# Optimization experiments

Hardware: AMD Instinct MI355X
Metric: run time of the kernel (lower is better)

Reference implementation:

```python
import jax, jax.numpy as jnp
import numpy as np

NEG_SLOPE = 0.2

def gat_conv(x, edge, W, att_src, att_dst, bias, heads, out_ch, concat):
    # x: [N, F_in], edge: [2, E] (self-loops already included)
    N = x.shape[0]
    src, dst = edge[0], edge[1]
    h = (x @ W).reshape(N, heads, out_ch)                     # [N, H, C]
    a_src = jnp.sum(h * att_src, axis=-1)                     # [N, H]
    a_dst = jnp.sum(h * att_dst, axis=-1)                     # [N, H]
    e = jax.nn.leaky_relu(a_src[src] + a_dst[dst], NEG_SLOPE)  # [E, H]
    # segment softmax over incoming edges of each dst node
    e_max = jax.ops.segment_max(e, dst, num_segments=N)       # [N, H]
    e_exp = jnp.exp(e - e_max[dst])                           # [E, H]
    denom = jax.ops.segment_sum(e_exp, dst, num_segments=N)   # [N, H]
    alpha = e_exp / denom[dst]                                # [E, H]
    msg = h[src] * alpha[:, :, None]                          # [E, H, C]
    out = jax.ops.segment_sum(msg, dst, num_segments=N)       # [N, H, C]
    if concat:
        out = out.reshape(N, heads * out_ch)
    else:
        out = out.mean(axis=1)
    return out + bias


def setup_inputs() -> dict:
    key = jax.random.key(0)
    ks = jax.random.split(key, 10)
    N, E = 50000, 1600000
    F_in, H, C1, n_cls = 256, 4, 64, 40
    x = jax.random.normal(ks[0], (N, F_in), dtype=jnp.float32)
    edge_index = jax.random.randint(ks[1], (2, E), 0, N, dtype=jnp.int64)
    s1 = 1.0 / np.sqrt(F_in)
    s2 = 1.0 / np.sqrt(H * C1)
    return {
        "x": x,
        "edge_index": edge_index,
        "W1": jax.random.normal(ks[2], (F_in, H * C1), dtype=jnp.float32) * s1,
        "att_src1": jax.random.normal(ks[3], (H, C1), dtype=jnp.float32) * s2,
        "att_dst1": jax.random.normal(ks[4], (H, C1), dtype=jnp.float32) * s2,
        "b1": jnp.zeros((H * C1,), dtype=jnp.float32),
        "W2": jax.random.normal(ks[5], (H * C1, n_cls), dtype=jnp.float32) * s2,
        "att_src2": jax.random.normal(ks[6], (1, n_cls), dtype=jnp.float32) * 0.1,
        "att_dst2": jax.random.normal(ks[7], (1, n_cls), dtype=jnp.float32) * 0.1,
        "b2": jnp.zeros((n_cls,), dtype=jnp.float32),
    }


def reference(x, edge_index, W1, att_src1, att_dst1, b1, W2, att_src2, att_dst2, b2):
    N = x.shape[0]
    # PyG GATConv adds self-loops by default
    loops = jnp.arange(N, dtype=edge_index.dtype)
    edge = jnp.concatenate([edge_index, jnp.stack([loops, loops])], axis=1)
    # dropout is identity in eval mode
    h = gat_conv(x, edge, W1, att_src1, att_dst1, b1, heads=4, out_ch=64, concat=True)
    h = jax.nn.elu(h)
    out = gat_conv(h, edge, W2, att_src2, att_dst2, b2, heads=1, out_ch=40, concat=False)
    return out
```

## Files before the change

### kernel.cpp

```cpp
#include <hip/hip_runtime.h>
#include <hip/hip_bf16.h>

typedef short bf16x8 __attribute__((ext_vector_type(8)));
typedef float f32x4 __attribute__((ext_vector_type(4)));
typedef float f32x2 __attribute__((ext_vector_type(2)));
typedef unsigned short u16x8 __attribute__((ext_vector_type(8)));

#define CHUNK 4096
#define BCAP 16384

__device__ __forceinline__ float wred_sum(float v) {
  #pragma unroll
  for (int off = 32; off > 0; off >>= 1)
    v += __shfl_xor(v, off, 64);
  return v;
}
__device__ __forceinline__ float b2f(unsigned short u) {
  union { unsigned int i; float f; } x;
  x.i = ((unsigned int)u) << 16;
  return x.f;
}
__device__ __forceinline__ unsigned short f2bu(float f) {
  __hip_bfloat16 b = __float2bfloat16(f);
  return *(unsigned short*)&b;
}
__device__ __forceinline__ void pkfma(f32x2& acc, f32x2 v, f32x2 w) {
  asm("v_pk_fma_f32 %0, %1, %2, %0" : "+v"(acc) : "v"(v), "v"(w));
}
__device__ __forceinline__ void qfma(f32x2* acc2, unsigned int u, f32x2 wp) {
  f32x2 a, b;
  a[0] = (float)(u & 0xFFu);         a[1] = (float)((u >> 8) & 0xFFu);
  b[0] = (float)((u >> 16) & 0xFFu); b[1] = (float)(u >> 24);
  pkfma(acc2[0], a, wp);
  pkfma(acc2[1], b, wp);
}
__device__ __forceinline__ void bffma(f32x2& acc, unsigned int up, f32x2 wp) {
  union { unsigned int i; float f; } lo, hi;
  lo.i = up << 16; hi.i = up & 0xFFFF0000u;
  f32x2 v; v[0] = lo.f; v[1] = hi.f;
  pkfma(acc, v, wp);
}
__device__ __forceinline__ float ldf(const void* p, long long i, int is16) {
  return is16 ? __bfloat162float(((const __hip_bfloat16*)p)[i])
              : ((const float*)p)[i];
}
__device__ __forceinline__ int edge_at(const int* e, long long idx, int is64) {
  return is64 ? (int)((const long long*)e)[idx] : e[idx];
}

__global__ void detect_kernel(const int* __restrict__ edge, int n_edge_check,
                              const unsigned int* __restrict__ xw, int n_x_check,
                              int* __restrict__ flag,
                              int* __restrict__ bcursor, int NB) {
  __shared__ int s_nz, s_cnt, s_tot;
  int tid = threadIdx.x;
  for (int b = tid; b < NB; b += 256) bcursor[b] = b * BCAP;
  if (tid == 0) { s_nz = 0; s_cnt = 0; s_tot = 0; }
  __syncthreads();
  int nz = 0;
  for (int k = tid; k < n_edge_check; k += 256)
    if (edge[2 * k + 1] != 0) nz = 1;
  if (nz) atomicOr(&s_nz, 1);
  int c = 0, t = 0;
  for (int k = tid; k < n_x_check; k += 256) {
    unsigned int w = xw[k];
    if (w == 0u) continue;
    t++;
    unsigned int e = (w >> 7) & 0xFFu;
    if (e >= 100u && e <= 150u) c++;
  }
  atomicAdd(&s_cnt, c);
  atomicAdd(&s_tot, t);
  __syncthreads();
  if (tid == 0) {
    flag[0] = (s_nz == 0) ? 1 : 0;
    flag[1] = (s_cnt * 10 > s_tot * 6) ? 1 : 0;
  }
}

__global__ __launch_bounds__(256) void partition_kernel(
    const int* __restrict__ edge, int E, int N, const int* __restrict__ flag,
    int* __restrict__ bcursor, unsigned int* __restrict__ part, int NB) {
  __shared__ int cnt[1024];
  __shared__ int loff[1025];
  __shared__ int gpos[1024];
  __shared__ int lcur[1024];
  __shared__ unsigned int staged[CHUNK];
  __shared__ int staged_addr[CHUNK];
  __shared__ int s[256];
  __shared__ int rbase;
  int tid = threadIdx.x;
  long long base = (long long)blockIdx.x * CHUNK;
  long long total = (long long)E + N;
  int maxa = NB * BCAP - 1;
  int here = (int)min((long long)CHUNK, total - base);
  for (int b = tid; b < NB; b += 256) cnt[b] = 0;
  if (tid == 0) rbase = 0;
  __syncthreads();
  int is64 = flag[0];
  int myb[16];
  unsigned int myp[16];
  #pragma unroll
  for (int j = 0; j < 16; j++) {
    long long i = base + j * 256 + tid;
    myb[j] = -1;
    if (i < total) {
      int d, sv;
      if (i < E) {
        sv = edge_at(edge, i, is64);
        d = edge_at(edge, (long long)E + i, is64);
      } else {
        sv = d = (int)(i - E);
      }
      d = min(max(d, 0), N - 1);
      sv = min(max(sv, 0), N - 1);
      myb[j] = d >> 8;
      myp[j] = ((unsigned int)(d & 255) << 24) | (unsigned int)sv;
      atomicAdd(&cnt[myb[j]], 1);
    }
  }
  __syncthreads();
  for (int c0 = 0; c0 < NB; c0 += 256) {
    int idx = c0 + tid;
    int v = (idx < NB) ? cnt[idx] : 0;
    s[tid] = v;
    __syncthreads();
    for (int off = 1; off < 256; off <<= 1) {
      int t = (tid >= off) ? s[tid - off] : 0;
      __syncthreads();
      s[tid] += t;
      __syncthreads();
    }
    int mb = rbase;
    if (idx < NB) loff[idx] = mb + s[tid] - v;
    __syncthreads();
    if (tid == 0) rbase = mb + s[255];
    __syncthreads();
  }
  __syncthreads();
  for (int b = tid; b < NB; b += 256) {
    int c = cnt[b];
    gpos[b] = c ? atomicAdd(&bcursor[b], c) : 0;
    lcur[b] = loff[b];
  }
  __syncthreads();
  #pragma unroll
  for (int j = 0; j < 16; j++) {
    if (myb[j] >= 0) {
      int b = myb[j];
      int slot = atomicAdd(&lcur[b], 1);
      staged[slot] = myp[j];
      staged_addr[slot] = min(gpos[b] + (slot - loff[b]), maxa);
    }
  }
  __syncthreads();
  for (int i = tid; i < here; i += 256)
    part[staged_addr[i]] = staged[i];
}

__global__ __launch_bounds__(256) void bucket_sort_kernel(
    const unsigned int* __restrict__ part, const int* __restrict__ bcursor,
    int N, int* __restrict__ indptr, int* __restrict__ iend,
    int* __restrict__ ssrc) {
  __shared__ int hist[256], cur[256];
  __shared__ int s[256];
  int tid = threadIdx.x;
  int b = blockIdx.x;
  int begin = b * BCAP, end = bcursor[b];
  hist[tid] = 0;
  __syncthreads();
  for (int i = begin + tid; i < end; i += 256)
    atomicAdd(&hist[part[i] >> 24], 1);
  __syncthreads();
  int v = hist[tid];
  s[tid] = v;
  __syncthreads();
  for (int off = 1; off < 256; off <<= 1) {
    int t = (tid >= off) ? s[tid - off] : 0;
    __syncthreads();
    s[tid] += t;
    __syncthreads();
  }
  int exc = s[tid] - v;
  cur[tid] = exc;
  int d = b * 256 + tid;
  if (d < N) { indptr[d] = begin + exc; iend[d] = begin + exc + v; }
  __syncthreads();
  for (int i = begin + tid; i < end; i += 256) {
    unsigned int p = part[i];
    int pos = begin + atomicAdd(&cur[p >> 24], 1);
    ssrc[pos] = (int)(p & 0xFFFFFFu);
  }
}

__global__ void prep_kernel(const void* __restrict__ x, __hip_bfloat16* __restrict__ xb,
                            long long n_valid4, long long nconv4,
                            const void* __restrict__ W1v, const void* __restrict__ W2v,
                            __hip_bfloat16* __restrict__ Wt1, __hip_bfloat16* __restrict__ Wt2,
                            int F, int HC, int C2, int C2p,
                            const int* __restrict__ dflag) {
  int f16 = dflag[1];
  long long i = blockIdx.x * 256LL + threadIdx.x;
  if (i < nconv4) {
    ushort4 o;
    if (i < n_valid4) {
      if (f16) {
        o = ((const ushort4*)x)[i];
      } else {
        float4 v = ((const float4*)x)[i];
        o.x = f2bu(v.x); o.y = f2bu(v.y); o.z = f2bu(v.z); o.w = f2bu(v.w);
      }
    } else {
      o.x = o.y = o.z = o.w = 0;
    }
    ((ushort4*)xb)[i] = o;
    return;
  }
  long long j = i - nconv4;
  int n1 = HC * F;
  if (j < n1) {
    int idx = (int)j;
    int n = idx / F, k = idx - n * F;
    Wt1[idx] = __float2bfloat16(ldf(W1v, (long long)k * HC + n, f16));
  } else {
    int jj = (int)(j - n1);
    if (jj >= C2p * HC) return;
    int n = jj / HC, k = jj - n * HC;
    float v = (n < C2) ? ldf(W2v, (long long)k * C2 + n, f16) : 0.f;
    Wt2[jj] = __float2bfloat16(v);
  }
}

__global__ __launch_bounds__(256) void mfma_gemm_kernel(
    const __hip_bfloat16* __restrict__ A, const __hip_bfloat16* __restrict__ BtT,
    __hip_bfloat16* __restrict__ Cb,
    const void* __restrict__ attS, const void* __restrict__ attD,
    float* __restrict__ aS, float* __restrict__ aD,
    float2* __restrict__ aSq, int att_stride,
    int M, int Nout, int K, int quant,
    unsigned char* __restrict__ h1q,
    const int* __restrict__ dflag) {
  int f16 = dflag[1];
  int tid = threadIdx.x;
  int w = tid >> 6, l = tid & 63;
  int m_lane = l & 15, q = l >> 4;
  int row0 = blockIdx.y * 64, col0 = blockIdx.x * 64;
  const __hip_bfloat16* Arow = A + (long long)(row0 + w * 16 + m_lane) * K + q * 8;
  const __hip_bfloat16* Brow = BtT + (long long)(col0 + m_lane) * K + q * 8;
  f32x4 acc[4] = {};
  #pragma unroll 4
  for (int k0 = 0; k0 < K; k0 += 32) {
    bf16x8 af = *(const bf16x8*)(Arow + k0);
    #pragma unroll
    for (int t = 0; t < 4; t++) {
      bf16x8 bf = *(const bf16x8*)(Brow + (long long)t * 16 * K + k0);
      acc[t] = __builtin_amdgcn_mfma_f32_16x16x32_bf16(af, bf, acc[t], 0, 0, 0);
    }
  }
  #pragma unroll
  for (int r = 0; r < 4; r++) {
    int gr = row0 + w * 16 + q * 4 + r;
    float ps = 0.f, pd = 0.f, vmax = 0.f;
    #pragma unroll
    for (int t = 0; t < 4; t++) {
      int gc = col0 + t * 16 + m_lane;
      float v = acc[t][r];
      if (gc < Nout) {
        ps += v * ldf(attS, gc, f16);
        pd += v * ldf(attD, gc, f16);
        vmax = fmaxf(vmax, fabsf(v));
        if (!quant && gr < M) Cb[(long long)gr * Nout + gc] = __float2bfloat16(v);
      }
    }
    #pragma unroll
    for (int off = 1; off < 16; off <<= 1) {
      ps += __shfl_xor(ps, off, 64);
      pd += __shfl_xor(pd, off, 64);
      vmax = fmaxf(vmax, __shfl_xor(vmax, off, 64));
    }
    if (quant && gr < M) {
      float qinv = (vmax > 0.f) ? 127.f / vmax : 0.f;
      #pragma unroll
      for (int t = 0; t < 4; t++) {
        int gc = col0 + t * 16 + m_lane;
        h1q[(long long)gr * 256 + gc] =
            (unsigned char)(__float2int_rn(acc[t][r] * qinv) + 128);
      }
      if (m_lane == 0) {
        float2 sq; sq.x = ps; sq.y = vmax * (1.f / 127.f);
        aSq[(long long)gr * att_stride + blockIdx.x] = sq;
      }
    }
    if (m_lane == 0 && gr < M) {
      if (!quant) aS[(long long)gr * att_stride + blockIdx.x] = ps;
      aD[(long long)gr * att_stride + blockIdx.x] = pd;
    }
  }
}

__global__ __launch_bounds__(256) void aggregate1_kernel(
    const int* __restrict__ indptr, const int* __restrict__ iend,
    const int* __restrict__ ssrc,
    const unsigned char* __restrict__ h1q, const float2* __restrict__ a_sq,
    const float* __restrict__ a_dst, const void* __restrict__ b1,
    __hip_bfloat16* __restrict__ h2b, int N, const int* __restrict__ dflag) {
  int f16 = dflag[1];
  int w = threadIdx.x >> 6, l = threadIdx.x & 63;
  int d = blockIdx.x * 4 + w;
  if (d >= N) return;
  int q = l >> 4;
  int e16 = l & 15;
  int hb = (l & 12) << 2;
  int chb = (l & 15) << 4;
  int begin = indptr[d], end = iend[d];
  float adst = a_dst[d * 4 + q];
  int s0 = ssrc[begin];
  float den = 0.f, accS = 0.f;
  f32x2 acc2[8] = {};
  for (int c = begin; c < end; c += 32) {
    int cnt = end - c;
    int sj0 = s0, sj1 = s0;
    float ws0 = 0.f, ws1 = 0.f;
    if (e16 < cnt) {
      sj0 = ssrc[c + e16];
      float2 t = a_sq[sj0 * 4 + q];
      float e = t.x + adst;
      e = (e > 0.f) ? e : 0.2f * e;
      float wj = __expf(e);
      den += wj; ws0 = wj * t.y;
    }
    if (e16 + 16 < cnt) {
      sj1 = ssrc[c + 16 + e16];
      float2 t = a_sq[sj1 * 4 + q];
      float e = t.x + adst;
      e = (e > 0.f) ? e : 0.2f * e;
      float wj = __expf(e);
      den += wj; ws1 = wj * t.y;
    }
    int m0 = cnt < 16 ? cnt : 16;
    int m1 = cnt - 16; m1 = m1 < 0 ? 0 : (m1 > 16 ? 16 : m1);
    int j0 = (m0 + 3) >> 2, j1 = (m1 + 3) >> 2;
    #pragma unroll 4
    for (int j = 0; j < j0; j++) {
      int idx = hb + 4 * j + q;
      int s = __shfl(sj0, idx, 64);
      float wt = __shfl(ws0, idx, 64);
      accS += wt;
      f32x2 wp; wp[0] = wt; wp[1] = wt;
      uint4 uv = *(const uint4*)(h1q + (long long)s * 256 + chb);
      qfma(&acc2[0], uv.x, wp);
      qfma(&acc2[2], uv.y, wp);
      qfma(&acc2[4], uv.z, wp);
      qfma(&acc2[6], uv.w, wp);
    }
    #pragma unroll 4
    for (int j = 0; j < j1; j++) {
      int idx = hb + 4 * j + q;
      int s = __shfl(sj1, idx, 64);
      float wt = __shfl(ws1, idx, 64);
      accS += wt;
      f32x2 wp; wp[0] = wt; wp[1] = wt;
      uint4 uv = *(const uint4*)(h1q + (long long)s * 256 + chb);
      qfma(&acc2[0], uv.x, wp);
      qfma(&acc2[2], uv.y, wp);
      qfma(&acc2[4], uv.z, wp);
      qfma(&acc2[6], uv.w, wp);
    }
  }
  float* af = (float*)acc2;
  #pragma unroll
  for (int i = 0; i < 16; i++) {
    af[i] += __shfl_xor(af[i], 16, 64);
    af[i] += __shfl_xor(af[i], 32, 64);
  }
  accS += __shfl_xor(accS, 16, 64);
  accS += __shfl_xor(accS, 32, 64);
  #pragma unroll
  for (int off = 1; off < 16; off <<= 1)
    den += __shfl_xor(den, off, 64);
  float deh = __shfl(den, hb, 64);
  float inv = 1.f / deh;
  if (l < 16) {
    u16x8 o0, o1;
    #pragma unroll
    for (int i = 0; i < 16; i++) {
      float v = (af[i] - 128.f * accS) * inv + ldf(b1, chb + i, f16);
      v = (v > 0.f) ? v : (__expf(v) - 1.f);
      if (i < 8) o0[i] = f2bu(v); else o1[i - 8] = f2bu(v);
    }
    u16x8* dst = (u16x8*)((unsigned short*)h2b + (long long)d * 256 + chb);
    dst[0] = o0;
    dst[1] = o1;
  }
}

__global__ __launch_bounds__(256) void aggregate2_kernel(
    const int* __restrict__ indptr, const int* __restrict__ iend,
    const int* __restrict__ ssrc,
    const __hip_bfloat16* __restrict__ gb, const float* __restrict__ a_src,
    const float* __restrict__ a_dst, const void* __restrict__ b2,
    void* __restrict__ out, int N, int C, const int* __restrict__ dflag) {
  int f16 = dflag[1];
  int w = threadIdx.x >> 6, l = threadIdx.x & 63;
  int d = blockIdx.x * 4 + w;
  if (d >= N) return;
  int begin = indptr[d], end = iend[d];
  float adst = a_dst[d];
  int eg = l / 10;
  int cq = l - eg * 10;
  bool act = (eg < 6);
  int s0 = ssrc[begin];
  float den = 0.f;
  f32x2 acc01 = {0.f, 0.f}, acc23 = {0.f, 0.f};
  for (int c = begin; c < end; c += 64) {
    int cnt = min(64, end - c);
    int sj = s0;
    float wj = 0.f;
    if (l < cnt) {
      sj = ssrc[c + l];
      float e = a_src[sj] + adst;
      e = (e > 0.f) ? e : 0.2f * e;
      wj = __expf(e);
    }
    den += wj;
    int jm = (cnt + 5) / 6;
    #pragma unroll 4
    for (int j = 0; j < jm; j++) {
      int idx = 6 * j + eg;
      int s = __shfl(sj, idx & 63, 64);
      float wt = __shfl(wj, idx & 63, 64);
      if (!act || idx >= cnt) wt = 0.f;
      uint2 gv = *(const uint2*)((const unsigned short*)gb +
                                 (long long)s * C + 4 * cq);
      f32x2 wp; wp[0] = wt; wp[1] = wt;
      bffma(acc01, gv.x, wp);
      bffma(acc23, gv.y, wp);
    }
  }
  den = wred_sum(den);
  float inv = 1.f / den;
  float a0 = acc01[0], a1 = acc01[1], a2 = acc23[0], a3 = acc23[1];
  #pragma unroll
  for (int k = 1; k < 6; k++) {
    int srcl = cq + 10 * k;
    a0 += __shfl(acc01[0], srcl, 64);
    a1 += __shfl(acc01[1], srcl, 64);
    a2 += __shfl(acc23[0], srcl, 64);
    a3 += __shfl(acc23[1], srcl, 64);
  }
  if (l < 10) {
    float v0 = a0 * inv + ldf(b2, 4 * l + 0, f16);
    float v1 = a1 * inv + ldf(b2, 4 * l + 1, f16);
    float v2 = a2 * inv + ldf(b2, 4 * l + 2, f16);
    float v3 = a3 * inv + ldf(b2, 4 * l + 3, f16);
    long long o = (long long)d * C + 4 * l;
    if (f16) {
      ushort4 ov;
      ov.x = f2bu(v0); ov.y = f2bu(v1); ov.z = f2bu(v2); ov.w = f2bu(v3);
      *(ushort4*)((unsigned short*)out + o) = ov;
    } else {
      float4 ov;
      ov.x = v0; ov.y = v1; ov.z = v2; ov.w = v3;
      *(float4*)((float*)out + o) = ov;
    }
  }
}

extern "C" void kernel_launch(void* const* d_in, const int* in_sizes, int n_in,
                              void* d_out, int out_size, void* d_ws, size_t ws_size,
                              hipStream_t stream) {
  const void* x   = d_in[0];
  const int* edge = (const int*)d_in[1];
  const void* W1  = d_in[2];
  const void* as1 = d_in[3];
  const void* ad1 = d_in[4];
  const void* b1  = d_in[5];
  const void* W2  = d_in[6];
  const void* as2 = d_in[7];
  const void* ad2 = d_in[8];
  const void* b2  = d_in[9];

  const int F  = 256;
  const int HC = 256;
  const int N  = in_sizes[0] / F;
  const int E  = in_sizes[1] / 2;
  const int C2 = in_sizes[9];
  const int C2p = 64;
  const int total = E + N;
  const int NB = (N + 255) / 256;
  const int Mpad = ((N + 63) / 64) * 64;

  char* p = (char*)d_ws;
  auto alloc = [&](size_t bytes) -> void* {
    void* r = (void*)p;
    p += (bytes + 255) & ~(size_t)255;
    return r;
  };
  __hip_bfloat16* xb  = (__hip_bfloat16*)alloc((size_t)Mpad * F * 2);
  unsigned char*  h1q = (unsigned char*)alloc((size_t)Mpad * HC);
  __hip_bfloat16* h2b = (__hip_bfloat16*)alloc((size_t)Mpad * HC * 2);
  __hip_bfloat16* gb  = (__hip_bfloat16*)alloc((size_t)Mpad * C2 * 2);
  __hip_bfloat16* Wt1 = (__hip_bfloat16*)alloc((size_t)HC * F * 2);
  __hip_bfloat16* Wt2 = (__hip_bfloat16*)alloc((size_t)C2p * HC * 2);
  float2* a_sq1 = (float2*)alloc((size_t)N * 4 * 8);
  float* a_dst1 = (float*)alloc((size_t)N * 4 * 4);
  float* a_src2 = (float*)alloc((size_t)N * 4);
  float* a_dst2 = (float*)alloc((size_t)N * 4);
  unsigned int* part = (unsigned int*)alloc((size_t)NB * BCAP * 4);
  int* ssrc     = (int*)alloc((size_t)NB * BCAP * 4);
  int* bcursor  = (int*)alloc((size_t)NB * 4);
  int* indptr   = (int*)alloc((size_t)(N + 1) * 4);
  int* iend     = (int*)alloc((size_t)N * 4);
  int* flag     = (int*)alloc(256);

  detect_kernel<<<1, 256, 0, stream>>>(edge, E < 2048 ? E : 2048,
                                       (const unsigned int*)x, 4096, flag,
                                       bcursor, NB);
  int nch = (total + CHUNK - 1) / CHUNK;
  partition_kernel<<<nch, 256, 0, stream>>>(edge, E, N, flag, bcursor, part, NB);
  bucket_sort_kernel<<<NB, 256, 0, stream>>>(part, bcursor, N, indptr, iend, ssrc);

  long long nconv4 = (long long)Mpad * F / 4;
  long long nprep = nconv4 + (long long)HC * F + (long long)C2p * HC;
  prep_kernel<<<(int)((nprep + 255) / 256), 256, 0, stream>>>(
      x, xb, (long long)N * F / 4, nconv4, W1, W2, Wt1, Wt2, F, HC, C2, C2p, flag);

  dim3 g1(HC / 64, Mpad / 64);
  mfma_gemm_kernel<<<g1, 256, 0, stream>>>(xb, Wt1, nullptr,
                                           as1, ad1, nullptr, a_dst1, a_sq1, 4,
                                           N, HC, F, 1, h1q, flag);
  aggregate1_kernel<<<(N + 3) / 4, 256, 0, stream>>>(indptr, iend, ssrc, h1q, a_sq1,
                                                     a_dst1, b1, h2b, N, flag);

  dim3 g2(1, Mpad / 64);
  mfma_gemm_kernel<<<g2, 256, 0, stream>>>(h2b, Wt2, gb,
                                           as2, ad2, a_src2, a_dst2, nullptr, 1,
                                           N, C2, HC, 0, nullptr, flag);
  aggregate2_kernel<<<(N + 3) / 4, 256, 0, stream>>>(indptr, iend, ssrc, gb, a_src2, a_dst2,
                                                     b2, d_out, N, C2, flag);
}
```

Baseline: 373.3 us.

## Replace bucket partition sort with atomic CSR build and fuse x conversion into GEMM

The two-pass bucket partition and bucket sort are replaced by three kernels: a global atomic degree count, a per-block scan with an atomic block base, and an atomic-cursor scatter of source indices. The separate fp32-to-bf16 conversion pass over x is removed, and the first GEMM now loads fp32 rows and converts them to bf16 in registers. This cuts a full read and write of x plus the intermediate partition buffer. In exchange it adds global atomics on hot destinations and reads edges twice, and the CSR order becomes nondeterministic because blocks claim scan offsets through an atomic rather than in block order.

```diff
diff --git a/kernel.cpp b/kernel.cpp
--- a/kernel.cpp
+++ b/kernel.cpp
@@ -7,7 +7,6 @@
 typedef unsigned short u16x8 __attribute__((ext_vector_type(8)));
 
 #define CHUNK 4096
-#define BCAP 16384
 
 __device__ __forceinline__ float wred_sum(float v) {
   #pragma unroll
@@ -50,11 +49,9 @@
 
 __global__ void detect_kernel(const int* __restrict__ edge, int n_edge_check,
                               const unsigned int* __restrict__ xw, int n_x_check,
-                              int* __restrict__ flag,
-                              int* __restrict__ bcursor, int NB) {
+                              int* __restrict__ flag) {
   __shared__ int s_nz, s_cnt, s_tot;
   int tid = threadIdx.x;
-  for (int b = tid; b < NB; b += 256) bcursor[b] = b * BCAP;
   if (tid == 0) { s_nz = 0; s_cnt = 0; s_tot = 0; }
   __syncthreads();
   int nz = 0;
@@ -78,32 +75,56 @@
   }
 }
 
-__global__ __launch_bounds__(256) void partition_kernel(
+__global__ __launch_bounds__(256) void count_kernel(
     const int* __restrict__ edge, int E, int N, const int* __restrict__ flag,
-    int* __restrict__ bcursor, unsigned int* __restrict__ part, int NB) {
-  __shared__ int cnt[1024];
-  __shared__ int loff[1025];
-  __shared__ int gpos[1024];
-  __shared__ int lcur[1024];
-  __shared__ unsigned int staged[CHUNK];
-  __shared__ int staged_addr[CHUNK];
-  __shared__ int s[256];
-  __shared__ int rbase;
+    int* __restrict__ deg) {
   int tid = threadIdx.x;
   long long base = (long long)blockIdx.x * CHUNK;
   long long total = (long long)E + N;
-  int maxa = NB * BCAP - 1;
-  int here = (int)min((long long)CHUNK, total - base);
-  for (int b = tid; b < NB; b += 256) cnt[b] = 0;
-  if (tid == 0) rbase = 0;
-  __syncthreads();
   int is64 = flag[0];
-  int myb[16];
-  unsigned int myp[16];
   #pragma unroll
   for (int j = 0; j < 16; j++) {
     long long i = base + j * 256 + tid;
-    myb[j] = -1;
+    if (i < total) {
+      int d = (i < E) ? edge_at(edge, (long long)E + i, is64) : (int)(i - E);
+      d = min(max(d, 0), N - 1);
+      atomicAdd(&deg[d], 1);
+    }
+  }
+}
+
+__global__ __launch_bounds__(256) void scan_kernel(
+    const int* __restrict__ deg, int N, int* __restrict__ gcur,
+    int* __restrict__ indptr, int* __restrict__ iend, int* __restrict__ cursor) {
+  __shared__ int s[256];
+  __shared__ int base;
+  int tid = threadIdx.x;
+  int d = blockIdx.x * 256 + tid;
+  int v = (d < N) ? deg[d] : 0;
+  s[tid] = v;
+  __syncthreads();
+  for (int off = 1; off < 256; off <<= 1) {
+    int t = (tid >= off) ? s[tid - off] : 0;
+    __syncthreads();
+    s[tid] += t;
+    __syncthreads();
+  }
+  if (tid == 255) base = atomicAdd(gcur, s[255]);
+  __syncthreads();
+  int exc = base + s[tid] - v;
+  if (d < N) { indptr[d] = exc; iend[d] = exc + v; cursor[d] = exc; }
+}
+
+__global__ __launch_bounds__(256) void scatter_kernel(
+    const int* __restrict__ edge, int E, int N, const int* __restrict__ flag,
+    int* __restrict__ cursor, int* __restrict__ ssrc) {
+  int tid = threadIdx.x;
+  long long base = (long long)blockIdx.x * CHUNK;
+  long long total = (long long)E + N;
+  int is64 = flag[0];
+  #pragma unroll
+  for (int j = 0; j < 16; j++) {
+    long long i = base + j * 256 + tid;
     if (i < total) {
       int d, sv;
       if (i < E) {
@@ -114,116 +135,24 @@
       }
       d = min(max(d, 0), N - 1);
       sv = min(max(sv, 0), N - 1);
-      myb[j] = d >> 8;
-      myp[j] = ((unsigned int)(d & 255) << 24) | (unsigned int)sv;
-      atomicAdd(&cnt[myb[j]], 1);
-    }
-  }
-  __syncthreads();
-  for (int c0 = 0; c0 < NB; c0 += 256) {
-    int idx = c0 + tid;
-    int v = (idx < NB) ? cnt[idx] : 0;
-    s[tid] = v;
-    __syncthreads();
-    for (int off = 1; off < 256; off <<= 1) {
-      int t = (tid >= off) ? s[tid - off] : 0;
-      __syncthreads();
-      s[tid] += t;
-      __syncthreads();
-    }
-    int mb = rbase;
-    if (idx < NB) loff[idx] = mb + s[tid] - v;
-    __syncthreads();
-    if (tid == 0) rbase = mb + s[255];
-    __syncthreads();
-  }
-  __syncthreads();
-  for (int b = tid; b < NB; b += 256) {
-    int c = cnt[b];
-    gpos[b] = c ? atomicAdd(&bcursor[b], c) : 0;
-    lcur[b] = loff[b];
-  }
-  __syncthreads();
-  #pragma unroll
-  for (int j = 0; j < 16; j++) {
-    if (myb[j] >= 0) {
-      int b = myb[j];
-      int slot = atomicAdd(&lcur[b], 1);
-      staged[slot] = myp[j];
-      staged_addr[slot] = min(gpos[b] + (slot - loff[b]), maxa);
-    }
-  }
-  __syncthreads();
-  for (int i = tid; i < here; i += 256)
-    part[staged_addr[i]] = staged[i];
-}
-
-__global__ __launch_bounds__(256) void bucket_sort_kernel(
-    const unsigned int* __restrict__ part, const int* __restrict__ bcursor,
-    int N, int* __restrict__ indptr, int* __restrict__ iend,
-    int* __restrict__ ssrc) {
-  __shared__ int hist[256], cur[256];
-  __shared__ int s[256];
-  int tid = threadIdx.x;
-  int b = blockIdx.x;
-  int begin = b * BCAP, end = bcursor[b];
-  hist[tid] = 0;
-  __syncthreads();
-  for (int i = begin + tid; i < end; i += 256)
-    atomicAdd(&hist[part[i] >> 24], 1);
-  __syncthreads();
-  int v = hist[tid];
-  s[tid] = v;
-  __syncthreads();
-  for (int off = 1; off < 256; off <<= 1) {
-    int t = (tid >= off) ? s[tid - off] : 0;
-    __syncthreads();
-    s[tid] += t;
-    __syncthreads();
-  }
-  int exc = s[tid] - v;
-  cur[tid] = exc;
-  int d = b * 256 + tid;
-  if (d < N) { indptr[d] = begin + exc; iend[d] = begin + exc + v; }
-  __syncthreads();
-  for (int i = begin + tid; i < end; i += 256) {
-    unsigned int p = part[i];
-    int pos = begin + atomicAdd(&cur[p >> 24], 1);
-    ssrc[pos] = (int)(p & 0xFFFFFFu);
-  }
-}
-
-__global__ void prep_kernel(const void* __restrict__ x, __hip_bfloat16* __restrict__ xb,
-                            long long n_valid4, long long nconv4,
-                            const void* __restrict__ W1v, const void* __restrict__ W2v,
+      int pos = atomicAdd(&cursor[d], 1);
+      ssrc[pos] = sv;
+    }
+  }
+}
+
+__global__ void prep_kernel(const void* __restrict__ W1v, const void* __restrict__ W2v,
                             __hip_bfloat16* __restrict__ Wt1, __hip_bfloat16* __restrict__ Wt2,
                             int F, int HC, int C2, int C2p,
                             const int* __restrict__ dflag) {
   int f16 = dflag[1];
-  long long i = blockIdx.x * 256LL + threadIdx.x;
-  if (i < nconv4) {
-    ushort4 o;
-    if (i < n_valid4) {
-      if (f16) {
-        o = ((const ushort4*)x)[i];
-      } else {
-        float4 v = ((const float4*)x)[i];
-        o.x = f2bu(v.x); o.y = f2bu(v.y); o.z = f2bu(v.z); o.w = f2bu(v.w);
-      }
-    } else {
-      o.x = o.y = o.z = o.w = 0;
-    }
-    ((ushort4*)xb)[i] = o;
-    return;
-  }
-  long long j = i - nconv4;
+  int i = blockIdx.x * 256 + threadIdx.x;
   int n1 = HC * F;
-  if (j < n1) {
-    int idx = (int)j;
-    int n = idx / F, k = idx - n * F;
-    Wt1[idx] = __float2bfloat16(ldf(W1v, (long long)k * HC + n, f16));
+  if (i < n1) {
+    int n = i / F, k = i - n * F;
+    Wt1[i] = __float2bfloat16(ldf(W1v, (long long)k * HC + n, f16));
   } else {
-    int jj = (int)(j - n1);
+    int jj = i - n1;
     if (jj >= C2p * HC) return;
     int n = jj / HC, k = jj - n * HC;
     float v = (n < C2) ? ldf(W2v, (long long)k * C2 + n, f16) : 0.f;
@@ -232,25 +161,41 @@
 }
 
 __global__ __launch_bounds__(256) void mfma_gemm_kernel(
-    const __hip_bfloat16* __restrict__ A, const __hip_bfloat16* __restrict__ BtT,
+    const void* __restrict__ A, const __hip_bfloat16* __restrict__ BtT,
     __hip_bfloat16* __restrict__ Cb,
     const void* __restrict__ attS, const void* __restrict__ attD,
     float* __restrict__ aS, float* __restrict__ aD,
     float2* __restrict__ aSq, int att_stride,
-    int M, int Nout, int K, int quant,
+    int M, int Nout, int K, int quant, int amode,
     unsigned char* __restrict__ h1q,
     const int* __restrict__ dflag) {
   int f16 = dflag[1];
+  int af16 = amode | f16;
   int tid = threadIdx.x;
   int w = tid >> 6, l = tid & 63;
   int m_lane = l & 15, q = l >> 4;
   int row0 = blockIdx.y * 64, col0 = blockIdx.x * 64;
-  const __hip_bfloat16* Arow = A + (long long)(row0 + w * 16 + m_lane) * K + q * 8;
+  int arow = row0 + w * 16 + m_lane;
+  bool aok = (arow < M);
+  const __hip_bfloat16* Ab = (const __hip_bfloat16*)A + (long long)arow * K + q * 8;
+  const float* Af = (const float*)A + (long long)arow * K + q * 8;
   const __hip_bfloat16* Brow = BtT + (long long)(col0 + m_lane) * K + q * 8;
   f32x4 acc[4] = {};
   #pragma unroll 4
   for (int k0 = 0; k0 < K; k0 += 32) {
-    bf16x8 af = *(const bf16x8*)(Arow + k0);
+    bf16x8 af = {};
+    if (aok) {
+      if (af16) {
+        af = *(const bf16x8*)(Ab + k0);
+      } else {
+        float4 u0 = *(const float4*)(Af + k0);
+        float4 u1 = *(const float4*)(Af + k0 + 4);
+        af[0] = (short)f2bu(u0.x); af[1] = (short)f2bu(u0.y);
+        af[2] = (short)f2bu(u0.z); af[3] = (short)f2bu(u0.w);
+        af[4] = (short)f2bu(u1.x); af[5] = (short)f2bu(u1.y);
+        af[6] = (short)f2bu(u1.z); af[7] = (short)f2bu(u1.w);
+      }
+    }
     #pragma unroll
     for (int t = 0; t < 4; t++) {
       bf16x8 bf = *(const bf16x8*)(Brow + (long long)t * 16 * K + k0);
@@ -496,7 +441,6 @@
     p += (bytes + 255) & ~(size_t)255;
     return r;
   };
-  __hip_bfloat16* xb  = (__hip_bfloat16*)alloc((size_t)Mpad * F * 2);
   unsigned char*  h1q = (unsigned char*)alloc((size_t)Mpad * HC);
   __hip_bfloat16* h2b = (__hip_bfloat16*)alloc((size_t)Mpad * HC * 2);
   __hip_bfloat16* gb  = (__hip_bfloat16*)alloc((size_t)Mpad * C2 * 2);
@@ -506,36 +450,37 @@
   float* a_dst1 = (float*)alloc((size_t)N * 4 * 4);
   float* a_src2 = (float*)alloc((size_t)N * 4);
   float* a_dst2 = (float*)alloc((size_t)N * 4);
-  unsigned int* part = (unsigned int*)alloc((size_t)NB * BCAP * 4);
-  int* ssrc     = (int*)alloc((size_t)NB * BCAP * 4);
-  int* bcursor  = (int*)alloc((size_t)NB * 4);
-  int* indptr   = (int*)alloc((size_t)(N + 1) * 4);
+  int* deg      = (int*)alloc((size_t)(N + 64) * 4);
+  int* gcur     = deg + N;
+  int* cursor   = (int*)alloc((size_t)N * 4);
+  int* indptr   = (int*)alloc((size_t)N * 4);
   int* iend     = (int*)alloc((size_t)N * 4);
+  int* ssrc     = (int*)alloc((size_t)total * 4);
   int* flag     = (int*)alloc(256);
 
+  hipMemsetAsync(deg, 0, (size_t)(N + 64) * 4, stream);
   detect_kernel<<<1, 256, 0, stream>>>(edge, E < 2048 ? E : 2048,
-                                       (const unsigned int*)x, 4096, flag,
-                                       bcursor, NB);
+                                       (const unsigned int*)x, 4096, flag);
   int nch = (total + CHUNK - 1) / CHUNK;
-  partition_kernel<<<nch, 256, 0, stream>>>(edge, E, N, flag, bcursor, part, NB);
-  bucket_sort_kernel<<<NB, 256, 0, stream>>>(part, bcursor, N, indptr, iend, ssrc);
-
-  long long nconv4 = (long long)Mpad * F / 4;
-  long long nprep = nconv4 + (long long)HC * F + (long long)C2p * HC;
-  prep_kernel<<<(int)((nprep + 255) / 256), 256, 0, stream>>>(
-      x, xb, (long long)N * F / 4, nconv4, W1, W2, Wt1, Wt2, F, HC, C2, C2p, flag);
+  count_kernel<<<nch, 256, 0, stream>>>(edge, E, N, flag, deg);
+  scan_kernel<<<NB, 256, 0, stream>>>(deg, N, gcur, indptr, iend, cursor);
+  scatter_kernel<<<nch, 256, 0, stream>>>(edge, E, N, flag, cursor, ssrc);
+
+  int nprep = HC * F + C2p * HC;
+  prep_kernel<<<(nprep + 255) / 256, 256, 0, stream>>>(
+      W1, W2, Wt1, Wt2, F, HC, C2, C2p, flag);
 
   dim3 g1(HC / 64, Mpad / 64);
-  mfma_gemm_kernel<<<g1, 256, 0, stream>>>(xb, Wt1, nullptr,
+  mfma_gemm_kernel<<<g1, 256, 0, stream>>>(x, Wt1, nullptr,
                                            as1, ad1, nullptr, a_dst1, a_sq1, 4,
-                                           N, HC, F, 1, h1q, flag);
+                                           N, HC, F, 1, 0, h1q, flag);
   aggregate1_kernel<<<(N + 3) / 4, 256, 0, stream>>>(indptr, iend, ssrc, h1q, a_sq1,
                                                      a_dst1, b1, h2b, N, flag);
 
   dim3 g2(1, Mpad / 64);
   mfma_gemm_kernel<<<g2, 256, 0, stream>>>(h2b, Wt2, gb,
                                            as2, ad2, a_src2, a_dst2, nullptr, 1,
-                                           N, C2, HC, 0, nullptr, flag);
+                                           N, C2, HC, 0, 1, nullptr, flag);
   aggregate2_kernel<<<(N + 3) / 4, 256, 0, stream>>>(indptr, iend, ssrc, gb, a_src2, a_dst2,
                                                      b2, d_out, N, C2, flag);
 }
```

Measured after the change: 533.2 us. 1.43x slower.
